# Kernel optimization log

Hardware: AMD Instinct MI355X
Metric: run time of the kernel (lower is better)

## Reference

```python
import jax, jax.numpy as jnp
import numpy as np

TOP_K = 2


def setup_inputs() -> dict:
    key = jax.random.key(0)
    kx, kw = jax.random.split(key)
    B, S, D, E = 4, 4096, 2048, 64
    x = jax.random.normal(kx, (B, S, D), dtype=jnp.float32)
    W = jax.random.normal(kw, (E, D), dtype=jnp.float32) * 0.02  # router weight [E, D]
    return {"x": x, "W": W}


def reference(x, W):
    B, S, D = x.shape
    E = W.shape[0]
    x_flat = x.reshape(-1, D)                      # [T, D], T = B*S
    router_logits = jnp.einsum('td,ed->te', x_flat, W)  # [T, E]
    router_probs = jax.nn.softmax(router_logits, axis=-1)
    expert_weights, expert_indices = jax.lax.top_k(router_probs, TOP_K)  # [T, K]
    expert_weights = expert_weights / jnp.sum(expert_weights, axis=-1, keepdims=True)
    expert_indices = expert_indices.reshape(B, S, TOP_K)
    expert_weights = expert_weights.reshape(B, S, TOP_K)
    # aux load-balance loss: sum((mean usage - 1/E)^2)
    expert_usage = jnp.mean(router_probs, axis=0)  # [E]
    aux_loss = jnp.sum((expert_usage - 1.0 / E) ** 2)
    return expert_indices, expert_weights, aux_loss
```

## Files before the change

kernel.cpp:

```cpp
#include <hip/hip_runtime.h>
#include <math.h>

#define T_TOK 16384
#define DDIM  2048
#define NE    64
#define NPLANE (NE * DDIM)
#define NBLK  512

typedef __attribute__((ext_vector_type(8))) short short8;
typedef __attribute__((ext_vector_type(4))) float floatx4;

union Frag8 { unsigned short u[8]; short8 v; };

__device__ __forceinline__ unsigned int bf16_rne_bits(float x) {
    unsigned int u = __builtin_bit_cast(unsigned int, x);
    return (u + 0x7fffu + ((u >> 16) & 1u)) & 0xffff0000u;
}

__device__ __forceinline__ void dma16(const float* g, float* lds) {
    __builtin_amdgcn_global_load_lds(
        (const __attribute__((address_space(1))) unsigned int*)g,
        (__attribute__((address_space(3))) unsigned int*)lds, 16, 0, 0);
}

__global__ void wsplit_kernel(const float* __restrict__ W,
                              unsigned short* __restrict__ wh,
                              unsigned short* __restrict__ wm,
                              unsigned short* __restrict__ wl) {
    int i = blockIdx.x * 256 + threadIdx.x;
    float w = W[i];
    unsigned int hb = bf16_rne_bits(w);
    float r  = w - __builtin_bit_cast(float, hb);
    unsigned int mb = bf16_rne_bits(r);
    float r2 = r - __builtin_bit_cast(float, mb);
    unsigned int lb = bf16_rne_bits(r2);
    wh[i] = (unsigned short)(hb >> 16);
    wm[i] = (unsigned short)(mb >> 16);
    wl[i] = (unsigned short)(lb >> 16);
}

__global__ __launch_bounds__(1024, 8)
void router_main(const float* __restrict__ x,
                 const unsigned short* __restrict__ wh,
                 const unsigned short* __restrict__ wm,
                 const unsigned short* __restrict__ wl,
                 float* __restrict__ out, float* __restrict__ usage_part) {
    __shared__ float As[2 * 8192];
    __shared__ float ured[16][NE];
    float* lg = As;

    const int tid  = threadIdx.x;
    const int lane = tid & 63;
    const int wv   = __builtin_amdgcn_readfirstlane(tid >> 6);
    const int nh   = wv & 1;
    const int kq   = wv >> 1;
    const int cl   = lane & 15;
    const int q    = lane >> 4;
    const int t0   = blockIdx.x * 32;

    const float* xdma = x + (size_t)(t0 + (lane & 31)) * DDIM + kq * 256 + (lane >> 5) * 4;

    floatx4 acc[2][2];
#pragma unroll
    for (int mt = 0; mt < 2; ++mt)
#pragma unroll
        for (int nt = 0; nt < 2; ++nt)
            acc[mt][nt] = (floatx4){0.f, 0.f, 0.f, 0.f};

    const size_t bbase = (size_t)(nh * 32 + cl) * DDIM + kq * 256 + q * 8;

#pragma unroll
    for (int g2 = 0; g2 < 2; ++g2) {
        const int g = nh * 2 + g2;
        dma16(xdma + g * 8, As + kq * 1024 + g * 256);
    }

#pragma unroll 1
    for (int c = 0; c < 8; ++c) {
        __syncthreads();

        if (c + 1 < 8) {
            float* nb = As + ((c + 1) & 1) * 8192 + kq * 1024;
#pragma unroll
            for (int g2 = 0; g2 < 2; ++g2) {
                const int g = nh * 2 + g2;
                dma16(xdma + (c + 1) * 32 + g * 8, nb + g * 256);
            }
        }

        const float* buf = As + (c & 1) * 8192 + kq * 1024;

        const size_t bo = bbase + c * 32;
        uint4 cb[2][3];
#pragma unroll
        for (int nt = 0; nt < 2; ++nt) {
            const size_t o = bo + (size_t)nt * 16 * DDIM;
            cb[nt][0] = *(const uint4*)(wh + o);
            cb[nt][1] = *(const uint4*)(wm + o);
            cb[nt][2] = *(const uint4*)(wl + o);
        }
        short8 Ah[2], Am[2], Al[2];
#pragma unroll
        for (int mt = 0; mt < 2; ++mt) {
            const float* ap = buf + q * 256 + (mt * 16 + cl) * 4;
            float4 a0 = *(const float4*)(ap);
            float4 a1 = *(const float4*)(ap + 128);
            float f[8] = {a0.x, a0.y, a0.z, a0.w, a1.x, a1.y, a1.z, a1.w};
            Frag8 fh, fm, fl;
#pragma unroll
            for (int j = 0; j < 8; ++j) {
                unsigned int ub = __builtin_bit_cast(unsigned int, f[j]);
                unsigned int hb = ub & 0xffff0000u;
                float r = f[j] - __builtin_bit_cast(float, hb);
                unsigned int rb = __builtin_bit_cast(unsigned int, r);
                unsigned int mb = rb & 0xffff0000u;
                float r2 = r - __builtin_bit_cast(float, mb);
                unsigned int lb = __builtin_bit_cast(unsigned int, r2);
                fh.u[j] = (unsigned short)(hb >> 16);
                fm.u[j] = (unsigned short)(mb >> 16);
                fl.u[j] = (unsigned short)(lb >> 16);
            }
            Ah[mt] = fh.v; Am[mt] = fm.v; Al[mt] = fl.v;
        }

#pragma unroll
        for (int mt = 0; mt < 2; ++mt)
#pragma unroll
            for (int nt = 0; nt < 2; ++nt) {
                short8 Bh = __builtin_bit_cast(short8, cb[nt][0]);
                short8 Bm = __builtin_bit_cast(short8, cb[nt][1]);
                short8 Bl = __builtin_bit_cast(short8, cb[nt][2]);
                floatx4 a = acc[mt][nt];
                a = __builtin_amdgcn_mfma_f32_16x16x32_bf16(Ah[mt], Bh, a, 0, 0, 0);
                a = __builtin_amdgcn_mfma_f32_16x16x32_bf16(Ah[mt], Bm, a, 0, 0, 0);
                a = __builtin_amdgcn_mfma_f32_16x16x32_bf16(Am[mt], Bh, a, 0, 0, 0);
                a = __builtin_amdgcn_mfma_f32_16x16x32_bf16(Am[mt], Bm, a, 0, 0, 0);
                a = __builtin_amdgcn_mfma_f32_16x16x32_bf16(Ah[mt], Bl, a, 0, 0, 0);
                a = __builtin_amdgcn_mfma_f32_16x16x32_bf16(Al[mt], Bh, a, 0, 0, 0);
                acc[mt][nt] = a;
            }
    }

    __syncthreads();

#pragma unroll
    for (int mt = 0; mt < 2; ++mt)
#pragma unroll
        for (int nt = 0; nt < 2; ++nt)
#pragma unroll
            for (int r = 0; r < 4; ++r)
                lg[kq * 2048 + (mt * 16 + q * 4 + r) * 64 + nh * 32 + nt * 16 + cl]
                    = acc[mt][nt][r];
    __syncthreads();

    float usage_acc = 0.f;
#pragma unroll 1
    for (int j = 0; j < 2; ++j) {
        const int tl = wv * 2 + j;
        const int t  = t0 + tl;
        float l = (((lg[0 * 2048 + tl * 64 + lane] + lg[1 * 2048 + tl * 64 + lane]) +
                    (lg[2 * 2048 + tl * 64 + lane] + lg[3 * 2048 + tl * 64 + lane])) +
                   ((lg[4 * 2048 + tl * 64 + lane] + lg[5 * 2048 + tl * 64 + lane]) +
                    (lg[6 * 2048 + tl * 64 + lane] + lg[7 * 2048 + tl * 64 + lane])));

        float v1 = l; int i1 = lane;
#pragma unroll
        for (int off = 32; off >= 1; off >>= 1) {
            float ov = __shfl_xor(v1, off, 64);
            int   oi = __shfl_xor(i1, off, 64);
            if (ov > v1 || (ov == v1 && oi < i1)) { v1 = ov; i1 = oi; }
        }
        float lm = (lane == i1) ? -INFINITY : l;
        float v2 = lm; int i2 = lane;
#pragma unroll
        for (int off = 32; off >= 1; off >>= 1) {
            float ov = __shfl_xor(v2, off, 64);
            int   oi = __shfl_xor(i2, off, 64);
            if (ov > v2 || (ov == v2 && oi < i2)) { v2 = ov; i2 = oi; }
        }

        float p = expf(l - v1);
        float s = p;
#pragma unroll
        for (int off = 32; off >= 1; off >>= 1) s += __shfl_xor(s, off, 64);

        float e2  = expf(v2 - v1);
        float rcp = 1.0f / (1.0f + e2);
        usage_acc += p / s;

        if (lane == 0) {
            out[(size_t)t * 2 + 0]         = (float)i1;
            out[(size_t)t * 2 + 1]         = (float)i2;
            out[32768 + (size_t)t * 2 + 0] = rcp;
            out[32768 + (size_t)t * 2 + 1] = e2 * rcp;
        }
    }

    ured[wv][lane] = usage_acc;
    __syncthreads();
    if (wv == 0) {
        float s = (((ured[0][lane] + ured[1][lane]) + (ured[2][lane] + ured[3][lane])) +
                   ((ured[4][lane] + ured[5][lane]) + (ured[6][lane] + ured[7][lane]))) +
                  (((ured[8][lane] + ured[9][lane]) + (ured[10][lane] + ured[11][lane])) +
                   ((ured[12][lane] + ured[13][lane]) + (ured[14][lane] + ured[15][lane])));
        usage_part[(size_t)blockIdx.x * 64 + lane] = s;
    }
}

__global__ __launch_bounds__(1024)
void router_aux(const float* __restrict__ usage_part, float* __restrict__ out) {
    __shared__ float red[16][NE];
    const int tid = threadIdx.x;
    const int e   = tid & 63;
    const int g   = tid >> 6;
    float s = 0.f;
#pragma unroll
    for (int i = 0; i < NBLK / 16; ++i)
        s += usage_part[(size_t)(g * (NBLK / 16) + i) * 64 + e];
    red[g][e] = s;
    __syncthreads();
    if (g == 0) {
        float tot = 0.f;
#pragma unroll
        for (int i = 0; i < 16; ++i) tot += red[i][e];
        float u = tot * (1.0f / 16384.0f) - (1.0f / 64.0f);
        float sq = u * u;
#pragma unroll
        for (int off = 32; off >= 1; off >>= 1) sq += __shfl_xor(sq, off, 64);
        if (e == 0) out[65536] = sq;
    }
}

extern "C" void kernel_launch(void* const* d_in, const int* in_sizes, int n_in,
                              void* d_out, int out_size, void* d_ws, size_t ws_size,
                              hipStream_t stream) {
    const float* x = (const float*)d_in[0];
    const float* W = (const float*)d_in[1];
    float* out     = (float*)d_out;

    unsigned short* ws_h = (unsigned short*)d_ws;
    unsigned short* ws_m = ws_h + NPLANE;
    unsigned short* ws_l = ws_m + NPLANE;
    float* upart         = (float*)(ws_l + NPLANE);

    wsplit_kernel<<<dim3(NPLANE / 256), dim3(256), 0, stream>>>(W, ws_h, ws_m, ws_l);
    router_main<<<dim3(NBLK), dim3(1024), 0, stream>>>(x, ws_h, ws_m, ws_l, out, upart);
    router_aux<<<dim3(1), dim3(1024), 0, stream>>>(upart, out);
}
```

Baseline: 240.2 us.

## Pre-swizzle router weights into fragment order and XOR-swizzle x tiles in LDS

The weight split kernel now writes the bf16 hi/mid/lo planes in MFMA fragment order, so each lane's B-fragment load in the main loop becomes one contiguous 16-byte read at a simple offset. The x DMA into LDS is reorganized so each wave copies whole token rows, with an XOR swizzle on the 16-byte column index to avoid LDS bank conflicts when fragments are read back. This is meant to improve global load coalescing and remove LDS bank conflicts and address arithmetic. The LDS layout and weight layout must stay consistent across both kernels.

```diff
diff --git a/kernel.cpp b/kernel.cpp
--- a/kernel.cpp
+++ b/kernel.cpp
@@ -27,8 +27,15 @@
                               unsigned short* __restrict__ wh,
                               unsigned short* __restrict__ wm,
                               unsigned short* __restrict__ wl) {
-    int i = blockIdx.x * 256 + threadIdx.x;
-    float w = W[i];
+    int i  = blockIdx.x * 256 + threadIdx.x;
+    int j  = i & 7;
+    int cl = (i >> 3) & 15;
+    int q  = (i >> 7) & 3;
+    int et = (i >> 9) & 3;
+    int kc = i >> 11;
+    int e  = et * 16 + cl;
+    int k  = kc * 32 + q * 8 + j;
+    float w = W[e * DDIM + k];
     unsigned int hb = bf16_rne_bits(w);
     float r  = w - __builtin_bit_cast(float, hb);
     unsigned int mb = bf16_rne_bits(r);
@@ -58,7 +65,9 @@
     const int q    = lane >> 4;
     const int t0   = blockIdx.x * 32;
 
-    const float* xdma = x + (size_t)(t0 + (lane & 31)) * DDIM + kq * 256 + (lane >> 5) * 4;
+    const int tlA0 = 2 * wv, tlA1 = 2 * wv + 1;
+    const float* ax0 = x + (size_t)(t0 + tlA0) * DDIM + ((lane ^ (tlA0 & 7)) << 2);
+    const float* ax1 = x + (size_t)(t0 + tlA1) * DDIM + ((lane ^ (tlA1 & 7)) << 2);
 
     floatx4 acc[2][2];
 #pragma unroll
@@ -67,44 +76,43 @@
         for (int nt = 0; nt < 2; ++nt)
             acc[mt][nt] = (floatx4){0.f, 0.f, 0.f, 0.f};
 
-    const size_t bbase = (size_t)(nh * 32 + cl) * DDIM + kq * 256 + q * 8;
-
-#pragma unroll
-    for (int g2 = 0; g2 < 2; ++g2) {
-        const int g = nh * 2 + g2;
-        dma16(xdma + g * 8, As + kq * 1024 + g * 256);
-    }
+    const unsigned lofs   = (unsigned)((q * 16 + cl) << 3);
+    const unsigned bfrag0 = ((unsigned)(kq * 4 + nh * 2 + 0) << 9) + lofs;
+    const unsigned bfrag1 = ((unsigned)(kq * 4 + nh * 2 + 1) << 9) + lofs;
+
+    dma16(ax0, As + tlA0 * 256);
+    dma16(ax1, As + tlA1 * 256);
 
 #pragma unroll 1
     for (int c = 0; c < 8; ++c) {
         __syncthreads();
 
         if (c + 1 < 8) {
-            float* nb = As + ((c + 1) & 1) * 8192 + kq * 1024;
-#pragma unroll
-            for (int g2 = 0; g2 < 2; ++g2) {
-                const int g = nh * 2 + g2;
-                dma16(xdma + (c + 1) * 32 + g * 8, nb + g * 256);
-            }
-        }
-
-        const float* buf = As + (c & 1) * 8192 + kq * 1024;
-
-        const size_t bo = bbase + c * 32;
+            float* nb = As + ((c + 1) & 1) * 8192;
+            dma16(ax0 + (c + 1) * 256, nb + tlA0 * 256);
+            dma16(ax1 + (c + 1) * 256, nb + tlA1 * 256);
+        }
+
+        const unsigned bo = (unsigned)c * 16384u;
         uint4 cb[2][3];
-#pragma unroll
-        for (int nt = 0; nt < 2; ++nt) {
-            const size_t o = bo + (size_t)nt * 16 * DDIM;
-            cb[nt][0] = *(const uint4*)(wh + o);
-            cb[nt][1] = *(const uint4*)(wm + o);
-            cb[nt][2] = *(const uint4*)(wl + o);
-        }
+        {
+            const unsigned o0 = bo + bfrag0, o1 = bo + bfrag1;
+            cb[0][0] = *(const uint4*)(wh + o0);
+            cb[0][1] = *(const uint4*)(wm + o0);
+            cb[0][2] = *(const uint4*)(wl + o0);
+            cb[1][0] = *(const uint4*)(wh + o1);
+            cb[1][1] = *(const uint4*)(wm + o1);
+            cb[1][2] = *(const uint4*)(wl + o1);
+        }
+
+        const float* buf = As + (c & 1) * 8192;
+        const int h0 = (kq * 8 + q * 2) ^ (cl & 7);
         short8 Ah[2], Am[2], Al[2];
 #pragma unroll
         for (int mt = 0; mt < 2; ++mt) {
-            const float* ap = buf + q * 256 + (mt * 16 + cl) * 4;
-            float4 a0 = *(const float4*)(ap);
-            float4 a1 = *(const float4*)(ap + 128);
+            const float* ap = buf + (mt * 16 + cl) * 256;
+            float4 a0 = *(const float4*)(ap + h0 * 4);
+            float4 a1 = *(const float4*)(ap + (h0 ^ 1) * 4);
             float f[8] = {a0.x, a0.y, a0.z, a0.w, a1.x, a1.y, a1.z, a1.w};
             Frag8 fh, fm, fl;
 #pragma unroll
```

New measurement: 232.6 us. -3.2%, faster.
